# Performance work log

Measured on AMD Instinct MI355X. Metric: run time of the kernel, lower is better.

The kernel has to match this reference:

```python
import jax, jax.numpy as jnp
import numpy as np

RNN = 1024     # rnn_size
POSE = 135     # config.pose_size (15 joints x 3x3 rotmat)
SEED = 120     # seed_seq_len
TGT = 24       # target_seq_len
B = 256        # batch size


def setup_inputs() -> dict:
    key = jax.random.key(0)
    k0, k1, k2, k3, k4 = jax.random.split(key, 5)
    s = 1.0 / np.sqrt(RNN)
    poses = jax.random.normal(k0, (B, SEED + TGT, POSE), dtype=jnp.float32)
    # nn.LSTMCell(input_size, rnn_size, bias=False): weights U(-1/sqrt(H), 1/sqrt(H))
    W_ih = jax.random.uniform(k1, (4 * RNN, POSE), minval=-s, maxval=s, dtype=jnp.float32)
    W_hh = jax.random.uniform(k2, (4 * RNN, RNN), minval=-s, maxval=s, dtype=jnp.float32)
    # nn.Linear(rnn_size, pose_size)
    W_fc = jax.random.uniform(k3, (POSE, RNN), minval=-s, maxval=s, dtype=jnp.float32)
    b_fc = jax.random.uniform(k4, (POSE,), minval=-s, maxval=s, dtype=jnp.float32)
    return {"poses": poses, "W_ih": W_ih, "W_hh": W_hh, "W_fc": W_fc, "b_fc": b_fc}


def reference(poses, W_ih, W_hh, W_fc, b_fc):
    def cell(x, h, c):
        # PyTorch LSTMCell gate order: i, f, g, o ; bias=False
        gates = x @ W_ih.T + h @ W_hh.T          # [B, 4*RNN]
        i, f, g, o = jnp.split(gates, 4, axis=-1)
        c_new = jax.nn.sigmoid(f) * c + jax.nn.sigmoid(i) * jnp.tanh(g)
        h_new = jax.nn.sigmoid(o) * jnp.tanh(c_new)
        return h_new, c_new

    # Encoder: steps over poses[:, 0:SEED-1] (dropout p=0 -> identity)
    enc_inputs = jnp.transpose(poses[:, : SEED - 1], (1, 0, 2))  # [SEED-1, B, POSE]
    h0 = jnp.zeros((B, RNN), dtype=poses.dtype)
    c0 = jnp.zeros((B, RNN), dtype=poses.dtype)

    def enc_step(carry, x):
        h, c = carry
        h, c = cell(x, h, c)
        return (h, c), None

    (h, c), _ = jax.lax.scan(enc_step, (h0, c0), enc_inputs)

    # first decoder input (poses[:, SEED-1]) is ground truth. inp is detached.
    inp0 = poses[:, SEED - 1]  # [B, POSE]

    def dec_step(carry, _):
        h, c, inp = carry
        inp = jax.lax.stop_gradient(inp)  # inp.detach() in the original
        h, c = cell(inp, h, c)
        out = inp + h @ W_fc.T + b_fc     # residual + linear decode
        return (h, c, out), out

    _, outs = jax.lax.scan(dec_step, (h, c, inp0), None, length=TGT)  # [TGT, B, POSE]
    return jnp.transpose(outs, (1, 0, 2))  # predictions [B, TGT, POSE]
```

## Files before the change

### kernel.cpp

```cpp
#include <hip/hip_runtime.h>
#include <stdint.h>

#define NB 256
#define NH 1024
#define NPOSE 135
#define NPPAD 160
#define NSTEPS 143
#define NDEC 24
#define KTOT 1184
#define LSTR 168
#define NWG 256

typedef __bf16 bf16;
typedef __attribute__((ext_vector_type(8))) __bf16 bf16x8;
typedef __attribute__((ext_vector_type(4))) float f32x4;
typedef __attribute__((ext_vector_type(4))) uint32_t u32x4;

#define WCAT_OFF 0
#define WCAT_BYTES (4096l * KTOT * 2)
#define WFC_OFF  (WCAT_OFF + WCAT_BYTES)
#define WFC_BYTES (144l * 1024 * 2)
#define X_OFF    (WFC_OFF + WFC_BYTES)
#define X_BYTES  (143l * NB * NPPAD * 2)
#define H_OFF    (X_OFF + X_BYTES)
#define H_BYTES2    (2l * NB * NH * 2)
#define H_BYTES144  (144l * NB * NH * 2)
#define BAR_BYTES 16384

__device__ __forceinline__ u32x4 llc_ld16(const void* p) {
  u32x4 v;
  asm volatile("global_load_dwordx4 %0, %1, off sc0 sc1"
               : "=v"(v) : "v"(p) : "memory");
  return v;
}
__device__ __forceinline__ u32x4 g_ld16(const void* p) {
  u32x4 v;
  asm volatile("global_load_dwordx4 %0, %1, off"
               : "=v"(v) : "v"(p) : "memory");
  return v;
}
__device__ __forceinline__ u32x4 ld16sel(const void* p, bool cached) {
  return cached ? g_ld16(p) : llc_ld16(p);
}
__device__ __forceinline__ void llc_st2(void* p, uint32_t v) {
  asm volatile("global_store_short %0, %1, off sc0 sc1"
               :: "v"(p), "v"(v) : "memory");
}
#define WAIT_VM(n) do { \
    asm volatile("s_waitcnt vmcnt(" #n ")" ::: "memory"); \
    __builtin_amdgcn_sched_barrier(0); } while (0)

#define POLL(ptr, tgt) do { \
    while (__hip_atomic_load((ptr), __ATOMIC_RELAXED, __HIP_MEMORY_SCOPE_AGENT) < (tgt)) \
      __builtin_amdgcn_s_sleep(1); \
  } while (0)
#define POLL_ALL8(tgt) do { \
    for (;;) { \
      int v_ = __hip_atomic_load(&bar[(bb * 8 + (lane & 7)) * 32], \
                                 __ATOMIC_RELAXED, __HIP_MEMORY_SCOPE_AGENT); \
      if (__all(v_ >= (tgt))) break; \
      __builtin_amdgcn_s_sleep(1); \
    } } while (0)

__global__ void k_zero(uint32_t* p, int n) {
  int i = blockIdx.x * blockDim.x + threadIdx.x;
  int st = gridDim.x * blockDim.x;
  for (; i < n; i += st) p[i] = 0u;
}

__global__ void k_wcat(const float* __restrict__ Whh, const float* __restrict__ Wih,
                       bf16* __restrict__ W) {
  int n = blockIdx.x;
  for (int kk = threadIdx.x; kk < KTOT; kk += blockDim.x) {
    float v = 0.f;
    if (kk < NH) v = Whh[(size_t)n * NH + kk];
    else if (kk - NH < NPOSE) v = Wih[(size_t)n * NPOSE + (kk - NH)];
    W[(size_t)n * KTOT + kk] = (bf16)v;
  }
}

__global__ void k_wfc(const float* __restrict__ Wfc, bf16* __restrict__ W) {
  int p = blockIdx.x;
  for (int kk = threadIdx.x; kk < NH; kk += blockDim.x) {
    float v = (p < NPOSE) ? Wfc[(size_t)p * NH + kk] : 0.f;
    W[(size_t)p * NH + kk] = (bf16)v;
  }
}

__global__ void k_x(const float* __restrict__ poses, bf16* __restrict__ X) {
  int idx = blockIdx.x;
  int t = idx >> 8, b = idx & 255;
  int p = threadIdx.x;
  if (p < NPPAD) {
    float v = (p < NPOSE) ? poses[((size_t)b * 144 + t) * NPOSE + p] : 0.f;
    X[(size_t)idx * NPPAD + p] = (bf16)v;
  }
}

__device__ __forceinline__ float sigm(float x) { return 1.f / (1.f + __expf(-x)); }
__device__ __forceinline__ float tanh_(float x) {
  float e = __expf(2.f * x);
  return 1.f - 2.f / (e + 1.f);
}

template <bool DEEP>
__global__ __launch_bounds__(256, 1) void
k_main(const float* __restrict__ poses, const float* __restrict__ bfc,
       const bf16* __restrict__ Wcat, const bf16* __restrict__ Wfcb,
       bf16* __restrict__ X, bf16* __restrict__ H, int* __restrict__ bar,
       float* __restrict__ out) {
  __shared__ bf16 BldsH[8 * 64 * 128];
  __shared__ bf16 BldsX[64 * LSTR];

  const int tid  = threadIdx.x;
  const int lane = tid & 63;
  const int wv   = tid >> 6;
  const int cl   = lane & 15;
  const int quad = lane >> 4;
  const int L    = blockIdx.x;
  const int jb = (L & 7) * 8 + ((L >> 3) & 7);
  const int bb = L >> 6;
  const int b0 = bb * 64;
  const int j0 = jb * 16;
  const int mych = jb >> 3;
  const bool is_out = ((L & 7) == 7) && (((L >> 3) & 7) < 4);
  const int brow0 = bb * 64 + ((L >> 3) & 7) * 16;

  for (int t = tid; t < 8 * 64 * 16; t += 256) {
    int c = t >> 10, rem = t & 1023, r = rem >> 4, xb = rem & 15;
    u32x4 v = *(const u32x4*)&Wcat[(size_t)((r >> 4) * NH + j0 + (r & 15)) * KTOT
                                   + c * 128 + xb * 8];
    *(u32x4*)&BldsH[(c * 64 + r) * 128 + ((xb ^ (r & 15)) << 3)] = v;
  }
  for (int it = 0; it < 5; ++it) {
    int u = tid + it * 256, r = u / 20, iu = u % 20;
    u32x4 v = *(const u32x4*)&Wcat[(size_t)((r >> 4) * NH + j0 + (r & 15)) * KTOT
                                   + 1024 + iu * 8];
    *(u32x4*)&BldsX[r * LSTR + iu * 8] = v;
  }
  __syncthreads();

  const int arow = b0 + wv * 16 + cl;
  const size_t aBase  = (size_t)arow * NH + quad * 8;
  const size_t axBase = (size_t)arow * NPPAD + quad * 8;

  u32x4 A0[4], A1[4], A2[4], AX[5];
  f32x4 acc[4];
  float cst[4] = {0.f, 0.f, 0.f, 0.f};

#define ISSUE_AH(SET, HP, chn) do { \
    const bf16* ga_ = (HP) + aBase + (chn) * 128; \
    SET[0] = ld16sel(ga_, DEEP);      SET[1] = ld16sel(ga_ + 32, DEEP); \
    SET[2] = ld16sel(ga_ + 64, DEEP); SET[3] = ld16sel(ga_ + 96, DEEP); } while (0)
#define ISSUE_AX(sv) do { \
    const bf16* ga_ = X + (size_t)(sv) * NB * NPPAD + axBase; \
    if ((sv) < 120) { \
      AX[0] = g_ld16(ga_);        AX[1] = g_ld16(ga_ + 32); \
      AX[2] = g_ld16(ga_ + 64);   AX[3] = g_ld16(ga_ + 96); \
      AX[4] = g_ld16(ga_ + 128); \
    } else { \
      AX[0] = ld16sel(ga_, DEEP);       AX[1] = ld16sel(ga_ + 32, DEEP); \
      AX[2] = ld16sel(ga_ + 64, DEEP);  AX[3] = ld16sel(ga_ + 96, DEEP); \
      AX[4] = ld16sel(ga_ + 128, DEEP); \
    } } while (0)
#define MFMA_LDS(SET, c) do { \
    _Pragma("unroll") \
    for (int ks = 0; ks < 4; ++ks) { \
      bf16x8 af_ = __builtin_bit_cast(bf16x8, SET[ks]); \
      _Pragma("unroll") \
      for (int gb = 0; gb < 4; ++gb) { \
        bf16x8 bw_ = *(const bf16x8*)&BldsH[((c) * 64 + gb * 16 + cl) * 128 \
                                            + (((ks * 4 + quad) ^ cl) << 3)]; \
        acc[gb] = __builtin_amdgcn_mfma_f32_16x16x32_bf16(af_, bw_, acc[gb], 0, 0, 0); \
      } } } while (0)
#define MFMA_X() do { \
    _Pragma("unroll") \
    for (int ks = 0; ks < 5; ++ks) { \
      bf16x8 af_ = __builtin_bit_cast(bf16x8, AX[ks]); \
      _Pragma("unroll") \
      for (int gb = 0; gb < 4; ++gb) { \
        bf16x8 bw_ = *(const bf16x8*)&BldsX[(gb * 16 + cl) * LSTR + ks * 32 + quad * 8]; \
        acc[gb] = __builtin_amdgcn_mfma_f32_16x16x32_bf16(af_, bw_, acc[gb], 0, 0, 0); \
      } } } while (0)

  ISSUE_AH(A0, H, 0);
  ISSUE_AH(A1, H, 1);

  for (int s = 0; s < NSTEPS; ++s) {
    const bf16* Hr = H + (size_t)(DEEP ? s : (s & 1)) * (NB * NH);
    bf16* Hw = H + (size_t)(DEEP ? (s + 1) : ((s + 1) & 1)) * (NB * NH);
    #pragma unroll
    for (int gb = 0; gb < 4; ++gb) acc[gb] = f32x4{0, 0, 0, 0};

    ISSUE_AH(A2, Hr, 2); WAIT_VM(8); MFMA_LDS(A0, 0);
    ISSUE_AH(A0, Hr, 3); WAIT_VM(8); MFMA_LDS(A1, 1);
    ISSUE_AH(A1, Hr, 4); WAIT_VM(8); MFMA_LDS(A2, 2);
    ISSUE_AH(A2, Hr, 5); WAIT_VM(8); MFMA_LDS(A0, 3);
    ISSUE_AH(A0, Hr, 6); WAIT_VM(8); MFMA_LDS(A1, 4);
    ISSUE_AH(A1, Hr, 7); WAIT_VM(8); MFMA_LDS(A2, 5);
    if (s >= 120) POLL(&bar[(32 + bb) * 32], 4 * (s - 119));
    ISSUE_AX(s);         WAIT_VM(9); MFMA_LDS(A0, 6);
                         WAIT_VM(5); MFMA_LDS(A1, 7);
                         WAIT_VM(0); MFMA_X();

    #pragma unroll
    for (int r = 0; r < 4; ++r) {
      float gi = sigm(acc[0][r]);
      float gf = sigm(acc[1][r]);
      float gg = tanh_(acc[2][r]);
      float go = sigm(acc[3][r]);
      float cn = gf * cst[r] + gi * gg;
      cst[r] = cn;
      float h = go * tanh_(cn);
      bf16 hb = (bf16)h;
      llc_st2(&Hw[(size_t)(b0 + wv * 16 + quad * 4 + r) * NH + j0 + cl],
              (uint32_t)__builtin_bit_cast(uint16_t, hb));
    }
    WAIT_VM(0);
    __syncthreads();
    if (tid == 0) atomicAdd(&bar[(bb * 8 + mych) * 32], 1);

    if (s >= 119 && is_out) {
      const int k = s - 119;
      POLL_ALL8(8 * (s + 1));
      f32x4 oa[3] = {{0,0,0,0},{0,0,0,0},{0,0,0,0}};
      const bf16* hrow = Hw + (size_t)(brow0 + cl) * NH;
      for (int kb = 0; kb < 4; ++kb) {
        u32x4 hv[8];
        #pragma unroll
        for (int t = 0; t < 8; ++t)
          hv[t] = ld16sel(&hrow[(kb * 8 + t) * 32 + quad * 8], DEEP);
        WAIT_VM(0);
        #pragma unroll
        for (int t = 0; t < 8; ++t) {
          bf16x8 af = __builtin_bit_cast(bf16x8, hv[t]);
          #pragma unroll
          for (int i = 0; i < 3; ++i) {
            int ct = wv + i * 4;
            if (ct > 8) continue;
            bf16x8 bw = *(const bf16x8*)&Wfcb[(size_t)(ct * 16 + cl) * NH
                                              + (kb * 8 + t) * 32 + quad * 8];
            oa[i] = __builtin_amdgcn_mfma_f32_16x16x32_bf16(af, bw, oa[i], 0, 0, 0);
          }
        }
      }
      #pragma unroll
      for (int i = 0; i < 3; ++i) {
        int ct = wv + i * 4;
        if (ct > 8) continue;
        int p = ct * 16 + cl;
        if (p < NPOSE) {
          #pragma unroll
          for (int r = 0; r < 4; ++r) {
            int b = brow0 + quad * 4 + r;
            float inp = (k == 0) ? poses[((size_t)b * 144 + 119) * NPOSE + p]
                                 : out[((size_t)b * NDEC + (k - 1)) * NPOSE + p];
            float v = oa[i][r] + inp + bfc[p];
            out[((size_t)b * NDEC + k) * NPOSE + p] = v;
            if (s + 1 < NSTEPS) {
              bf16 xb = (bf16)v;
              llc_st2(&X[((size_t)(s + 1) * NB + b) * NPPAD + p],
                      (uint32_t)__builtin_bit_cast(uint16_t, xb));
            }
          }
        }
      }
      if (s + 1 < NSTEPS) {
        WAIT_VM(0);
        __syncthreads();
        if (tid == 0) atomicAdd(&bar[(32 + bb) * 32], 1);
      }
    }

    if (s + 1 < NSTEPS) {
      POLL_ALL8(8 * (s + 1));
      ISSUE_AH(A0, Hw, 0);
      ISSUE_AH(A1, Hw, 1);
    }
  }
}

extern "C" void kernel_launch(void* const* d_in, const int* in_sizes, int n_in,
                              void* d_out, int out_size, void* d_ws, size_t ws_size,
                              hipStream_t stream) {
  const float* poses = (const float*)d_in[0];
  const float* Wih   = (const float*)d_in[1];
  const float* Whh   = (const float*)d_in[2];
  const float* Wfc   = (const float*)d_in[3];
  const float* bfc   = (const float*)d_in[4];

  const size_t need_deep = (size_t)H_OFF + H_BYTES144 + BAR_BYTES;
  const size_t need_min  = (size_t)H_OFF + H_BYTES2 + BAR_BYTES;
  if (ws_size < need_min) return;
  const bool deep = ws_size >= need_deep;
  const size_t hbytes = deep ? (size_t)H_BYTES144 : (size_t)H_BYTES2;

  char* ws = (char*)d_ws;
  bf16* Wcat = (bf16*)(ws + WCAT_OFF);
  bf16* Wfcb = (bf16*)(ws + WFC_OFF);
  bf16* X    = (bf16*)(ws + X_OFF);
  bf16* H    = (bf16*)(ws + H_OFF);
  int*  bar  = (int*)(ws + H_OFF + hbytes);

  if (deep) {
    k_zero<<<256, 256, 0, stream>>>((uint32_t*)(ws + H_OFF), (int)(NB * NH * 2 / 4));
    k_zero<<<32, 256, 0, stream>>>((uint32_t*)bar, BAR_BYTES / 4);
  } else {
    k_zero<<<256, 256, 0, stream>>>((uint32_t*)(ws + H_OFF),
                                    (int)((H_BYTES2 + BAR_BYTES) / 4));
  }
  k_zero<<<256, 256, 0, stream>>>((uint32_t*)(X + (size_t)120 * NB * NPPAD),
                                  (int)(23l * NB * NPPAD * 2 / 4));
  k_wcat<<<4096, 256, 0, stream>>>(Whh, Wih, Wcat);
  k_wfc<<<144, 256, 0, stream>>>(Wfc, Wfcb);
  k_x<<<120 * 256, 256, 0, stream>>>(poses, X);
  if (deep)
    k_main<true><<<NWG, 256, 0, stream>>>(poses, bfc, Wcat, Wfcb, X, H, bar,
                                          (float*)d_out);
  else
    k_main<false><<<NWG, 256, 0, stream>>>(poses, bfc, Wcat, Wfcb, X, H, bar,
                                           (float*)d_out);
}
```

Measured before the change: 1.610 ms.

## Split K across wave pairs with LDS reduction and per-chunk barrier polling

Each wave now computes two 16-row batch tiles over half of the hidden-state K chunks, with the weight fragment as the A operand. Partial accumulators are exchanged through shared memory in four synchronized phases. Only the first half-waves run the LSTM gate math, and they write h as packed 8-byte stores instead of 2-byte shorts. Barrier polling is narrowed so each wave half waits only on the producer chunks it reads next, which lets it start prefetching sooner. The cost is extra __syncthreads, LDS traffic, and idle gate-math waves, while the per-step MFMA load is redistributed across waves.

Result: slower. 1.978 ms (+22.8%).

```diff
diff --git a/kernel.cpp b/kernel.cpp
--- a/kernel.cpp
+++ b/kernel.cpp
@@ -15,6 +15,7 @@
 typedef __attribute__((ext_vector_type(8))) __bf16 bf16x8;
 typedef __attribute__((ext_vector_type(4))) float f32x4;
 typedef __attribute__((ext_vector_type(4))) uint32_t u32x4;
+typedef __attribute__((ext_vector_type(2))) uint32_t u32x2;
 
 #define WCAT_OFF 0
 #define WCAT_BYTES (4096l * KTOT * 2)
@@ -42,8 +43,8 @@
 __device__ __forceinline__ u32x4 ld16sel(const void* p, bool cached) {
   return cached ? g_ld16(p) : llc_ld16(p);
 }
-__device__ __forceinline__ void llc_st2(void* p, uint32_t v) {
-  asm volatile("global_store_short %0, %1, off sc0 sc1"
+__device__ __forceinline__ void llc_st8(void* p, u32x2 v) {
+  asm volatile("global_store_dwordx2 %0, %1, off sc0 sc1"
                :: "v"(p), "v"(v) : "memory");
 }
 #define WAIT_VM(n) do { \
@@ -54,9 +55,9 @@
     while (__hip_atomic_load((ptr), __ATOMIC_RELAXED, __HIP_MEMORY_SCOPE_AGENT) < (tgt)) \
       __builtin_amdgcn_s_sleep(1); \
   } while (0)
-#define POLL_ALL8(tgt) do { \
+#define POLL_SET(cidx, tgt) do { \
     for (;;) { \
-      int v_ = __hip_atomic_load(&bar[(bb * 8 + (lane & 7)) * 32], \
+      int v_ = __hip_atomic_load(&bar[(bb * 8 + (cidx)) * 32], \
                                  __ATOMIC_RELAXED, __HIP_MEMORY_SCOPE_AGENT); \
       if (__all(v_ >= (tgt))) break; \
       __builtin_amdgcn_s_sleep(1); \
@@ -102,6 +103,11 @@
   float e = __expf(2.f * x);
   return 1.f - 2.f / (e + 1.f);
 }
+__device__ __forceinline__ uint32_t pack2(float a, float b) {
+  uint16_t lo = __builtin_bit_cast(uint16_t, (bf16)a);
+  uint16_t hi = __builtin_bit_cast(uint16_t, (bf16)b);
+  return ((uint32_t)hi << 16) | lo;
+}
 
 template <bool DEEP>
 __global__ __launch_bounds__(256, 1) void
@@ -111,13 +117,16 @@
        float* __restrict__ out) {
   __shared__ bf16 BldsH[8 * 64 * 128];
   __shared__ bf16 BldsX[64 * LSTR];
-
-  const int tid  = threadIdx.x;
-  const int lane = tid & 63;
-  const int wv   = tid >> 6;
-  const int cl   = lane & 15;
-  const int quad = lane >> 4;
-  const int L    = blockIdx.x;
+  __shared__ float XCH[2][64][20];
+
+  const int tid   = threadIdx.x;
+  const int lane  = tid & 63;
+  const int wv    = tid >> 6;
+  const int cl    = lane & 15;
+  const int quad  = lane >> 4;
+  const int khalf = wv >> 1;
+  const int bpair = wv & 1;
+  const int L  = blockIdx.x;
   const int jb = (L & 7) * 8 + ((L >> 3) & 7);
   const int bb = L >> 6;
   const int b0 = bb * 64;
@@ -140,89 +149,130 @@
   }
   __syncthreads();
 
-  const int arow = b0 + wv * 16 + cl;
-  const size_t aBase  = (size_t)arow * NH + quad * 8;
-  const size_t axBase = (size_t)arow * NPPAD + quad * 8;
-
-  u32x4 A0[4], A1[4], A2[4], AX[5];
-  f32x4 acc[4];
-  float cst[4] = {0.f, 0.f, 0.f, 0.f};
-
-#define ISSUE_AH(SET, HP, chn) do { \
-    const bf16* ga_ = (HP) + aBase + (chn) * 128; \
-    SET[0] = ld16sel(ga_, DEEP);      SET[1] = ld16sel(ga_ + 32, DEEP); \
-    SET[2] = ld16sel(ga_ + 64, DEEP); SET[3] = ld16sel(ga_ + 96, DEEP); } while (0)
-#define ISSUE_AX(sv) do { \
-    const bf16* ga_ = X + (size_t)(sv) * NB * NPPAD + axBase; \
+  const int arow0 = b0 + bpair * 32 + cl;
+  const size_t hB0 = (size_t)arow0 * NH + quad * 8;
+  const size_t hB1 = hB0 + (size_t)16 * NH;
+  const size_t xB0 = (size_t)arow0 * NPPAD + quad * 8;
+  const size_t xB1 = xB0 + (size_t)16 * NPPAD;
+
+  u32x4 B0[8], B1[8], B2[8], BX[10];
+  f32x4 acc[2][4];
+  float cst[8];
+  #pragma unroll
+  for (int r = 0; r < 8; ++r) cst[r] = 0.f;
+
+#define ISSUE_B(SET, HP, chn) do { \
+    const bf16* g0_ = (HP) + hB0 + (chn) * 128; \
+    const bf16* g1_ = (HP) + hB1 + (chn) * 128; \
+    SET[0] = ld16sel(g0_, DEEP);      SET[1] = ld16sel(g0_ + 32, DEEP); \
+    SET[2] = ld16sel(g0_ + 64, DEEP); SET[3] = ld16sel(g0_ + 96, DEEP); \
+    SET[4] = ld16sel(g1_, DEEP);      SET[5] = ld16sel(g1_ + 32, DEEP); \
+    SET[6] = ld16sel(g1_ + 64, DEEP); SET[7] = ld16sel(g1_ + 96, DEEP); } while (0)
+#define ISSUE_BX(sv) do { \
+    const bf16* g0_ = X + (size_t)(sv) * NB * NPPAD + xB0; \
+    const bf16* g1_ = X + (size_t)(sv) * NB * NPPAD + xB1; \
     if ((sv) < 120) { \
-      AX[0] = g_ld16(ga_);        AX[1] = g_ld16(ga_ + 32); \
-      AX[2] = g_ld16(ga_ + 64);   AX[3] = g_ld16(ga_ + 96); \
-      AX[4] = g_ld16(ga_ + 128); \
+      _Pragma("unroll") \
+      for (int k_ = 0; k_ < 5; ++k_) { BX[k_] = g_ld16(g0_ + k_ * 32); \
+                                       BX[5 + k_] = g_ld16(g1_ + k_ * 32); } \
     } else { \
-      AX[0] = ld16sel(ga_, DEEP);       AX[1] = ld16sel(ga_ + 32, DEEP); \
-      AX[2] = ld16sel(ga_ + 64, DEEP);  AX[3] = ld16sel(ga_ + 96, DEEP); \
-      AX[4] = ld16sel(ga_ + 128, DEEP); \
+      _Pragma("unroll") \
+      for (int k_ = 0; k_ < 5; ++k_) { BX[k_] = ld16sel(g0_ + k_ * 32, DEEP); \
+                                       BX[5 + k_] = ld16sel(g1_ + k_ * 32, DEEP); } \
     } } while (0)
-#define MFMA_LDS(SET, c) do { \
+#define MFMA_H(SET, c) do { \
     _Pragma("unroll") \
     for (int ks = 0; ks < 4; ++ks) { \
-      bf16x8 af_ = __builtin_bit_cast(bf16x8, SET[ks]); \
+      bf16x8 h0_ = __builtin_bit_cast(bf16x8, SET[ks]); \
+      bf16x8 h1_ = __builtin_bit_cast(bf16x8, SET[4 + ks]); \
       _Pragma("unroll") \
-      for (int gb = 0; gb < 4; ++gb) { \
-        bf16x8 bw_ = *(const bf16x8*)&BldsH[((c) * 64 + gb * 16 + cl) * 128 \
+      for (int gt = 0; gt < 4; ++gt) { \
+        bf16x8 wf_ = *(const bf16x8*)&BldsH[((c) * 64 + gt * 16 + cl) * 128 \
                                             + (((ks * 4 + quad) ^ cl) << 3)]; \
-        acc[gb] = __builtin_amdgcn_mfma_f32_16x16x32_bf16(af_, bw_, acc[gb], 0, 0, 0); \
+        acc[0][gt] = __builtin_amdgcn_mfma_f32_16x16x32_bf16(wf_, h0_, acc[0][gt], 0, 0, 0); \
+        acc[1][gt] = __builtin_amdgcn_mfma_f32_16x16x32_bf16(wf_, h1_, acc[1][gt], 0, 0, 0); \
       } } } while (0)
 #define MFMA_X() do { \
     _Pragma("unroll") \
     for (int ks = 0; ks < 5; ++ks) { \
-      bf16x8 af_ = __builtin_bit_cast(bf16x8, AX[ks]); \
+      bf16x8 h0_ = __builtin_bit_cast(bf16x8, BX[ks]); \
+      bf16x8 h1_ = __builtin_bit_cast(bf16x8, BX[5 + ks]); \
       _Pragma("unroll") \
-      for (int gb = 0; gb < 4; ++gb) { \
-        bf16x8 bw_ = *(const bf16x8*)&BldsX[(gb * 16 + cl) * LSTR + ks * 32 + quad * 8]; \
-        acc[gb] = __builtin_amdgcn_mfma_f32_16x16x32_bf16(af_, bw_, acc[gb], 0, 0, 0); \
+      for (int gt = 0; gt < 4; ++gt) { \
+        bf16x8 wf_ = *(const bf16x8*)&BldsX[(gt * 16 + cl) * LSTR + ks * 32 + quad * 8]; \
+        acc[0][gt] = __builtin_amdgcn_mfma_f32_16x16x32_bf16(wf_, h0_, acc[0][gt], 0, 0, 0); \
+        acc[1][gt] = __builtin_amdgcn_mfma_f32_16x16x32_bf16(wf_, h1_, acc[1][gt], 0, 0, 0); \
       } } } while (0)
 
-  ISSUE_AH(A0, H, 0);
-  ISSUE_AH(A1, H, 1);
+  if (khalf == 0) { ISSUE_B(B0, H, 0); ISSUE_B(B1, H, 1); }
+  else            { ISSUE_B(B0, H, 5); ISSUE_B(B1, H, 6); }
 
   for (int s = 0; s < NSTEPS; ++s) {
     const bf16* Hr = H + (size_t)(DEEP ? s : (s & 1)) * (NB * NH);
     bf16* Hw = H + (size_t)(DEEP ? (s + 1) : ((s + 1) & 1)) * (NB * NH);
     #pragma unroll
-    for (int gb = 0; gb < 4; ++gb) acc[gb] = f32x4{0, 0, 0, 0};
-
-    ISSUE_AH(A2, Hr, 2); WAIT_VM(8); MFMA_LDS(A0, 0);
-    ISSUE_AH(A0, Hr, 3); WAIT_VM(8); MFMA_LDS(A1, 1);
-    ISSUE_AH(A1, Hr, 4); WAIT_VM(8); MFMA_LDS(A2, 2);
-    ISSUE_AH(A2, Hr, 5); WAIT_VM(8); MFMA_LDS(A0, 3);
-    ISSUE_AH(A0, Hr, 6); WAIT_VM(8); MFMA_LDS(A1, 4);
-    ISSUE_AH(A1, Hr, 7); WAIT_VM(8); MFMA_LDS(A2, 5);
-    if (s >= 120) POLL(&bar[(32 + bb) * 32], 4 * (s - 119));
-    ISSUE_AX(s);         WAIT_VM(9); MFMA_LDS(A0, 6);
-                         WAIT_VM(5); MFMA_LDS(A1, 7);
-                         WAIT_VM(0); MFMA_X();
-
-    #pragma unroll
-    for (int r = 0; r < 4; ++r) {
-      float gi = sigm(acc[0][r]);
-      float gf = sigm(acc[1][r]);
-      float gg = tanh_(acc[2][r]);
-      float go = sigm(acc[3][r]);
-      float cn = gf * cst[r] + gi * gg;
-      cst[r] = cn;
-      float h = go * tanh_(cn);
-      bf16 hb = (bf16)h;
-      llc_st2(&Hw[(size_t)(b0 + wv * 16 + quad * 4 + r) * NH + j0 + cl],
-              (uint32_t)__builtin_bit_cast(uint16_t, hb));
-    }
-    WAIT_VM(0);
+    for (int bt = 0; bt < 2; ++bt)
+      #pragma unroll
+      for (int gt = 0; gt < 4; ++gt) acc[bt][gt] = f32x4{0, 0, 0, 0};
+
+    if (khalf == 0) {
+      ISSUE_B(B2, Hr, 2); WAIT_VM(16); MFMA_H(B0, 0);
+      ISSUE_B(B0, Hr, 3); WAIT_VM(16); MFMA_H(B1, 1);
+      ISSUE_B(B1, Hr, 4); WAIT_VM(16); MFMA_H(B2, 2);
+                          WAIT_VM(8);  MFMA_H(B0, 3);
+                          WAIT_VM(0);  MFMA_H(B1, 4);
+    } else {
+      ISSUE_B(B2, Hr, 7); WAIT_VM(16); MFMA_H(B0, 5);
+      if (s >= 120) POLL(&bar[(32 + bb) * 32], 4 * (s - 119));
+      ISSUE_BX(s);        WAIT_VM(18); MFMA_H(B1, 6);
+                          WAIT_VM(10); MFMA_H(B2, 7);
+                          WAIT_VM(0);  MFMA_X();
+      #pragma unroll
+      for (int gt = 0; gt < 4; ++gt)
+        *(f32x4*)&XCH[bpair][lane][gt * 4] = acc[0][gt];
+    }
     __syncthreads();
-    if (tid == 0) atomicAdd(&bar[(bb * 8 + mych) * 32], 1);
+    if (khalf == 0) {
+      #pragma unroll
+      for (int gt = 0; gt < 4; ++gt)
+        acc[0][gt] += *(const f32x4*)&XCH[bpair][lane][gt * 4];
+    }
+    __syncthreads();
+    if (khalf == 1) {
+      #pragma unroll
+      for (int gt = 0; gt < 4; ++gt)
+        *(f32x4*)&XCH[bpair][lane][gt * 4] = acc[1][gt];
+    }
+    __syncthreads();
+    if (khalf == 0) {
+      #pragma unroll
+      for (int gt = 0; gt < 4; ++gt)
+        acc[1][gt] += *(const f32x4*)&XCH[bpair][lane][gt * 4];
+    }
+    __syncthreads();
+
+    if (khalf == 0) {
+      #pragma unroll
+      for (int bt = 0; bt < 2; ++bt) {
+        float hv[4];
+        #pragma unroll
+        for (int r = 0; r < 4; ++r) {
+          float iv = acc[bt][0][r], fv = acc[bt][1][r];
+          float gv = acc[bt][2][r], ov = acc[bt][3][r];
+          float cn = sigm(fv) * cst[bt * 4 + r] + sigm(iv) * tanh_(gv);
+          cst[bt * 4 + r] = cn;
+          hv[r] = sigm(ov) * tanh_(cn);
+        }
+        u32x2 pk; pk[0] = pack2(hv[0], hv[1]); pk[1] = pack2(hv[2], hv[3]);
+        llc_st8(&Hw[(size_t)(arow0 + bt * 16) * NH + j0 + quad * 4], pk);
+      }
+      WAIT_VM(0);
+      if (lane == 0) atomicAdd(&bar[(bb * 8 + mych) * 32], 1);
+    }
 
     if (s >= 119 && is_out) {
       const int k = s - 119;
-      POLL_ALL8(8 * (s + 1));
+      POLL_SET(lane & 7, 16 * (s + 1));
       f32x4 oa[3] = {{0,0,0,0},{0,0,0,0},{0,0,0,0}};
       const bf16* hrow = Hw + (size_t)(brow0 + cl) * NH;
       for (int kb = 0; kb < 4; ++kb) {
@@ -259,8 +309,9 @@
             out[((size_t)b * NDEC + k) * NPOSE + p] = v;
             if (s + 1 < NSTEPS) {
               bf16 xb = (bf16)v;
-              llc_st2(&X[((size_t)(s + 1) * NB + b) * NPPAD + p],
-                      (uint32_t)__builtin_bit_cast(uint16_t, xb));
+              asm volatile("global_store_short %0, %1, off sc0 sc1"
+                           :: "v"(&X[((size_t)(s + 1) * NB + b) * NPPAD + p]),
+                              "v"((uint32_t)__builtin_bit_cast(uint16_t, xb)) : "memory");
             }
           }
         }
@@ -273,9 +324,16 @@
     }
 
     if (s + 1 < NSTEPS) {
-      POLL_ALL8(8 * (s + 1));
-      ISSUE_AH(A0, Hw, 0);
-      ISSUE_AH(A1, Hw, 1);
+      bf16* Hn = H + (size_t)(DEEP ? (s + 1) : ((s + 1) & 1)) * (NB * NH);
+      if (khalf == 0) {
+        int c = lane & 7; if (c > 4) c = 0;
+        POLL_SET(c, 16 * (s + 1));
+        ISSUE_B(B0, Hn, 0); ISSUE_B(B1, Hn, 1);
+      } else {
+        int c = 5 + (lane % 3);
+        POLL_SET(c, 16 * (s + 1));
+        ISSUE_B(B0, Hn, 5); ISSUE_B(B1, Hn, 6);
+      }
     }
   }
 }
```

## Switch LSTM gate GEMM to 32x32x16 MFMA with cross-wave gate exchange

Applied to the files above, without the earlier changes.

Replaces the per-wave 16x16x32 MFMA tiling (each wave covering 16 batch rows and all four gates) with 32x32x16 MFMAs. Each wave now covers 32 batch rows and two gate blocks. Gate pairs are exchanged through a small LDS buffer with an extra __syncthreads, and the cell update is done by half the waves. The aim is fewer MFMA issues and fewer LDS B-operand reads per step, but it doubles the A-register footprint, adds a block barrier per step, and serializes the nonlinearities onto two waves. The H store hint also drops sc0, which changes cache coherence behaviour for the cross-workgroup exchange.

Result: slower. 2.305 ms (+43.1%).

```diff
diff --git a/kernel.cpp b/kernel.cpp
--- a/kernel.cpp
+++ b/kernel.cpp
@@ -14,6 +14,7 @@
 typedef __bf16 bf16;
 typedef __attribute__((ext_vector_type(8))) __bf16 bf16x8;
 typedef __attribute__((ext_vector_type(4))) float f32x4;
+typedef __attribute__((ext_vector_type(16))) float f32x16;
 typedef __attribute__((ext_vector_type(4))) uint32_t u32x4;
 
 #define WCAT_OFF 0
@@ -43,7 +44,7 @@
   return cached ? g_ld16(p) : llc_ld16(p);
 }
 __device__ __forceinline__ void llc_st2(void* p, uint32_t v) {
-  asm volatile("global_store_short %0, %1, off sc0 sc1"
+  asm volatile("global_store_short %0, %1, off sc1"
                :: "v"(p), "v"(v) : "memory");
 }
 #define WAIT_VM(n) do { \
@@ -111,12 +112,19 @@
        float* __restrict__ out) {
   __shared__ bf16 BldsH[8 * 64 * 128];
   __shared__ bf16 BldsX[64 * LSTR];
+  __shared__ float XCH[2 * 64 * 18];
 
   const int tid  = threadIdx.x;
   const int lane = tid & 63;
   const int wv   = tid >> 6;
+  const int lrow = lane & 31;
+  const int half = lane >> 5;
+  const int l15  = lane & 15;
   const int cl   = lane & 15;
   const int quad = lane >> 4;
+  const int bt   = wv & 1;
+  const int ct   = wv >> 1;
+  const int ct32 = ct * 32;
   const int L    = blockIdx.x;
   const int jb = (L & 7) * 8 + ((L >> 3) & 7);
   const int bb = L >> 6;
@@ -140,48 +148,44 @@
   }
   __syncthreads();
 
-  const int arow = b0 + wv * 16 + cl;
-  const size_t aBase  = (size_t)arow * NH + quad * 8;
-  const size_t axBase = (size_t)arow * NPPAD + quad * 8;
-
-  u32x4 A0[4], A1[4], A2[4], AX[5];
-  f32x4 acc[4];
-  float cst[4] = {0.f, 0.f, 0.f, 0.f};
+  const int arow = b0 + 32 * bt + lrow;
+  const size_t aBase  = (size_t)arow * NH + half * 8;
+  const size_t axBase = (size_t)arow * NPPAD + half * 8;
+
+  u32x4 A0[8], A1[8], A2[8], AX[10];
+  f32x16 acc;
+  float cst[8];
+  #pragma unroll
+  for (int r = 0; r < 8; ++r) cst[r] = 0.f;
 
 #define ISSUE_AH(SET, HP, chn) do { \
     const bf16* ga_ = (HP) + aBase + (chn) * 128; \
-    SET[0] = ld16sel(ga_, DEEP);      SET[1] = ld16sel(ga_ + 32, DEEP); \
-    SET[2] = ld16sel(ga_ + 64, DEEP); SET[3] = ld16sel(ga_ + 96, DEEP); } while (0)
+    _Pragma("unroll") \
+    for (int kk_ = 0; kk_ < 8; ++kk_) SET[kk_] = ld16sel(ga_ + kk_ * 16, DEEP); } while (0)
 #define ISSUE_AX(sv) do { \
     const bf16* ga_ = X + (size_t)(sv) * NB * NPPAD + axBase; \
     if ((sv) < 120) { \
-      AX[0] = g_ld16(ga_);        AX[1] = g_ld16(ga_ + 32); \
-      AX[2] = g_ld16(ga_ + 64);   AX[3] = g_ld16(ga_ + 96); \
-      AX[4] = g_ld16(ga_ + 128); \
+      _Pragma("unroll") \
+      for (int kk_ = 0; kk_ < 10; ++kk_) AX[kk_] = g_ld16(ga_ + kk_ * 16); \
     } else { \
-      AX[0] = ld16sel(ga_, DEEP);       AX[1] = ld16sel(ga_ + 32, DEEP); \
-      AX[2] = ld16sel(ga_ + 64, DEEP);  AX[3] = ld16sel(ga_ + 96, DEEP); \
-      AX[4] = ld16sel(ga_ + 128, DEEP); \
+      _Pragma("unroll") \
+      for (int kk_ = 0; kk_ < 10; ++kk_) AX[kk_] = ld16sel(ga_ + kk_ * 16, DEEP); \
     } } while (0)
-#define MFMA_LDS(SET, c) do { \
+#define MFMA_H32(SET, c) do { \
     _Pragma("unroll") \
-    for (int ks = 0; ks < 4; ++ks) { \
-      bf16x8 af_ = __builtin_bit_cast(bf16x8, SET[ks]); \
-      _Pragma("unroll") \
-      for (int gb = 0; gb < 4; ++gb) { \
-        bf16x8 bw_ = *(const bf16x8*)&BldsH[((c) * 64 + gb * 16 + cl) * 128 \
-                                            + (((ks * 4 + quad) ^ cl) << 3)]; \
-        acc[gb] = __builtin_amdgcn_mfma_f32_16x16x32_bf16(af_, bw_, acc[gb], 0, 0, 0); \
-      } } } while (0)
-#define MFMA_X() do { \
+    for (int kk_ = 0; kk_ < 8; ++kk_) { \
+      bf16x8 af_ = __builtin_bit_cast(bf16x8, SET[kk_]); \
+      bf16x8 bw_ = *(const bf16x8*)&BldsH[((c) * 64 + ct32 + lrow) * 128 \
+                                          + (((kk_ * 2 + half) ^ l15) << 3)]; \
+      acc = __builtin_amdgcn_mfma_f32_32x32x16_bf16(af_, bw_, acc, 0, 0, 0); \
+    } } while (0)
+#define MFMA_X32() do { \
     _Pragma("unroll") \
-    for (int ks = 0; ks < 5; ++ks) { \
-      bf16x8 af_ = __builtin_bit_cast(bf16x8, AX[ks]); \
-      _Pragma("unroll") \
-      for (int gb = 0; gb < 4; ++gb) { \
-        bf16x8 bw_ = *(const bf16x8*)&BldsX[(gb * 16 + cl) * LSTR + ks * 32 + quad * 8]; \
-        acc[gb] = __builtin_amdgcn_mfma_f32_16x16x32_bf16(af_, bw_, acc[gb], 0, 0, 0); \
-      } } } while (0)
+    for (int kk_ = 0; kk_ < 10; ++kk_) { \
+      bf16x8 af_ = __builtin_bit_cast(bf16x8, AX[kk_]); \
+      bf16x8 bw_ = *(const bf16x8*)&BldsX[(ct32 + lrow) * LSTR + kk_ * 16 + half * 8]; \
+      acc = __builtin_amdgcn_mfma_f32_32x32x16_bf16(af_, bw_, acc, 0, 0, 0); \
+    } } while (0)
 
   ISSUE_AH(A0, H, 0);
   ISSUE_AH(A1, H, 1);
@@ -189,34 +193,54 @@
   for (int s = 0; s < NSTEPS; ++s) {
     const bf16* Hr = H + (size_t)(DEEP ? s : (s & 1)) * (NB * NH);
     bf16* Hw = H + (size_t)(DEEP ? (s + 1) : ((s + 1) & 1)) * (NB * NH);
+    acc = (f32x16)(0.f);
+
+    ISSUE_AH(A2, Hr, 2); WAIT_VM(16); MFMA_H32(A0, 0);
+    ISSUE_AH(A0, Hr, 3); WAIT_VM(16); MFMA_H32(A1, 1);
+    ISSUE_AH(A1, Hr, 4); WAIT_VM(16); MFMA_H32(A2, 2);
+    ISSUE_AH(A2, Hr, 5); WAIT_VM(16); MFMA_H32(A0, 3);
+    ISSUE_AH(A0, Hr, 6); WAIT_VM(16); MFMA_H32(A1, 4);
+    ISSUE_AH(A1, Hr, 7); WAIT_VM(16); MFMA_H32(A2, 5);
+    if (s >= 120) POLL(&bar[(32 + bb) * 32], 4 * (s - 119));
+    ISSUE_AX(s);         WAIT_VM(18); MFMA_H32(A0, 6);
+                         WAIT_VM(10); MFMA_H32(A1, 7);
+                         WAIT_VM(0);  MFMA_X32();
+
+    float va[8], vb[8];
     #pragma unroll
-    for (int gb = 0; gb < 4; ++gb) acc[gb] = f32x4{0, 0, 0, 0};
-
-    ISSUE_AH(A2, Hr, 2); WAIT_VM(8); MFMA_LDS(A0, 0);
-    ISSUE_AH(A0, Hr, 3); WAIT_VM(8); MFMA_LDS(A1, 1);
-    ISSUE_AH(A1, Hr, 4); WAIT_VM(8); MFMA_LDS(A2, 2);
-    ISSUE_AH(A2, Hr, 5); WAIT_VM(8); MFMA_LDS(A0, 3);
-    ISSUE_AH(A0, Hr, 6); WAIT_VM(8); MFMA_LDS(A1, 4);
-    ISSUE_AH(A1, Hr, 7); WAIT_VM(8); MFMA_LDS(A2, 5);
-    if (s >= 120) POLL(&bar[(32 + bb) * 32], 4 * (s - 119));
-    ISSUE_AX(s);         WAIT_VM(9); MFMA_LDS(A0, 6);
-                         WAIT_VM(5); MFMA_LDS(A1, 7);
-                         WAIT_VM(0); MFMA_X();
-
-    #pragma unroll
-    for (int r = 0; r < 4; ++r) {
-      float gi = sigm(acc[0][r]);
-      float gf = sigm(acc[1][r]);
-      float gg = tanh_(acc[2][r]);
-      float go = sigm(acc[3][r]);
-      float cn = gf * cst[r] + gi * gg;
-      cst[r] = cn;
-      float h = go * tanh_(cn);
-      bf16 hb = (bf16)h;
-      llc_st2(&Hw[(size_t)(b0 + wv * 16 + quad * 4 + r) * NH + j0 + cl],
-              (uint32_t)__builtin_bit_cast(uint16_t, hb));
-    }
-    WAIT_VM(0);
+    for (int r8i = 0; r8i < 8; ++r8i) {
+      float sa = __shfl_xor(acc[r8i], 16);
+      float sb = __shfl_xor(acc[r8i + 8], 16);
+      const bool lo = (lrow < 16);
+      va[r8i] = lo ? acc[r8i] : sb;
+      vb[r8i] = lo ? sa : acc[r8i + 8];
+    }
+    const int xbase = (bt * 64 + lane) * 18;
+    if (ct == 1) {
+      #pragma unroll
+      for (int r8i = 0; r8i < 8; ++r8i) {
+        XCH[xbase + r8i * 2]     = tanh_(va[r8i]);
+        XCH[xbase + r8i * 2 + 1] = sigm(vb[r8i]);
+      }
+    }
+    __syncthreads();
+
+    if (ct == 0) {
+      #pragma unroll
+      for (int r8i = 0; r8i < 8; ++r8i) {
+        float tg = XCH[xbase + r8i * 2];
+        float so = XCH[xbase + r8i * 2 + 1];
+        float cn = sigm(vb[r8i]) * cst[r8i] + sigm(va[r8i]) * tg;
+        cst[r8i] = cn;
+        float h = so * tanh_(cn);
+        int reg = (lrow < 16) ? r8i : (r8i + 8);
+        int row32 = (reg & 3) + 8 * (reg >> 2) + 4 * half;
+        bf16 hb = (bf16)h;
+        llc_st2(&Hw[(size_t)(b0 + 32 * bt + row32) * NH + j0 + l15],
+                (uint32_t)__builtin_bit_cast(uint16_t, hb));
+      }
+      WAIT_VM(0);
+    }
     __syncthreads();
     if (tid == 0) atomicAdd(&bar[(bb * 8 + mych) * 32], 1);
 
@@ -236,9 +260,9 @@
           bf16x8 af = __builtin_bit_cast(bf16x8, hv[t]);
           #pragma unroll
           for (int i = 0; i < 3; ++i) {
-            int ct = wv + i * 4;
-            if (ct > 8) continue;
-            bf16x8 bw = *(const bf16x8*)&Wfcb[(size_t)(ct * 16 + cl) * NH
+            int ctd = wv + i * 4;
+            if (ctd > 8) continue;
+            bf16x8 bw = *(const bf16x8*)&Wfcb[(size_t)(ctd * 16 + cl) * NH
                                               + (kb * 8 + t) * 32 + quad * 8];
             oa[i] = __builtin_amdgcn_mfma_f32_16x16x32_bf16(af, bw, oa[i], 0, 0, 0);
           }
@@ -246,9 +270,9 @@
       }
       #pragma unroll
       for (int i = 0; i < 3; ++i) {
-        int ct = wv + i * 4;
-        if (ct > 8) continue;
-        int p = ct * 16 + cl;
+        int ctd = wv + i * 4;
+        if (ctd > 8) continue;
+        int p = ctd * 16 + cl;
         if (p < NPOSE) {
           #pragma unroll
           for (int r = 0; r < 4; ++r) {
```

## Replace full step barrier with per-chunk readiness flags checked lazily

Applied to the files above, without the earlier changes.

Before, each step waited for all 8 producer chunks of the new hidden state before loading any of it. Now, in the deep-buffer path, it waits only for chunks 0 and 1. It then prefetches each later chunk's flag with an LLC-coherent load and checks it just before issuing that chunk's loads, so early MFMA work overlaps with peers still writing later chunks. This adds extra flag loads and poll loops into the MFMA pipeline and reshuffles the vmcnt waits, which could cost latency or add ordering risk. The double-buffer fallback still uses the full barrier.

Result: faster. 1.558 ms (-3.2%).

```diff
diff --git a/kernel.cpp b/kernel.cpp
--- a/kernel.cpp
+++ b/kernel.cpp
@@ -33,6 +33,12 @@
                : "=v"(v) : "v"(p) : "memory");
   return v;
 }
+__device__ __forceinline__ uint32_t llc_ld4(const void* p) {
+  uint32_t v;
+  asm volatile("global_load_dword %0, %1, off sc0 sc1"
+               : "=v"(v) : "v"(p) : "memory");
+  return v;
+}
 __device__ __forceinline__ u32x4 g_ld16(const void* p) {
   u32x4 v;
   asm volatile("global_load_dwordx4 %0, %1, off"
@@ -60,6 +66,19 @@
                                  __ATOMIC_RELAXED, __HIP_MEMORY_SCOPE_AGENT); \
       if (__all(v_ >= (tgt))) break; \
       __builtin_amdgcn_s_sleep(1); \
+    } } while (0)
+#define POLL01(tgt) do { \
+    for (;;) { \
+      int v_ = __hip_atomic_load(&bar[(bb * 8 + (lane & 1)) * 32], \
+                                 __ATOMIC_RELAXED, __HIP_MEMORY_SCOPE_AGENT); \
+      if (__all(v_ >= (tgt))) break; \
+      __builtin_amdgcn_s_sleep(1); \
+    } } while (0)
+#define CHK(fv, ch, tgt) do { \
+    while ((int)(fv) < (tgt)) { \
+      __builtin_amdgcn_s_sleep(1); \
+      fv = llc_ld4(&bar[(bb * 8 + (ch)) * 32]); \
+      WAIT_VM(0); \
     } } while (0)
 
 __global__ void k_zero(uint32_t* p, int n) {
@@ -145,9 +164,11 @@
   const size_t axBase = (size_t)arow * NPPAD + quad * 8;
 
   u32x4 A0[4], A1[4], A2[4], AX[5];
+  uint32_t f2 = 0, f3 = 0, f4 = 0, f5 = 0, f6 = 0, f7 = 0;
   f32x4 acc[4];
   float cst[4] = {0.f, 0.f, 0.f, 0.f};
 
+#define FLAGP(ch) (&bar[(bb * 8 + (ch)) * 32])
 #define ISSUE_AH(SET, HP, chn) do { \
     const bf16* ga_ = (HP) + aBase + (chn) * 128; \
     SET[0] = ld16sel(ga_, DEEP);      SET[1] = ld16sel(ga_ + 32, DEEP); \
@@ -183,25 +204,27 @@
         acc[gb] = __builtin_amdgcn_mfma_f32_16x16x32_bf16(af_, bw_, acc[gb], 0, 0, 0); \
       } } } while (0)
 
-  ISSUE_AH(A0, H, 0);
-  ISSUE_AH(A1, H, 1);
+  ISSUE_AH(A0, H, 0);  f2 = llc_ld4(FLAGP(2));
+  ISSUE_AH(A1, H, 1);  f3 = llc_ld4(FLAGP(3));
 
   for (int s = 0; s < NSTEPS; ++s) {
     const bf16* Hr = H + (size_t)(DEEP ? s : (s & 1)) * (NB * NH);
     bf16* Hw = H + (size_t)(DEEP ? (s + 1) : ((s + 1) & 1)) * (NB * NH);
     #pragma unroll
     for (int gb = 0; gb < 4; ++gb) acc[gb] = f32x4{0, 0, 0, 0};
-
-    ISSUE_AH(A2, Hr, 2); WAIT_VM(8); MFMA_LDS(A0, 0);
-    ISSUE_AH(A0, Hr, 3); WAIT_VM(8); MFMA_LDS(A1, 1);
-    ISSUE_AH(A1, Hr, 4); WAIT_VM(8); MFMA_LDS(A2, 2);
-    ISSUE_AH(A2, Hr, 5); WAIT_VM(8); MFMA_LDS(A0, 3);
-    ISSUE_AH(A0, Hr, 6); WAIT_VM(8); MFMA_LDS(A1, 4);
-    ISSUE_AH(A1, Hr, 7); WAIT_VM(8); MFMA_LDS(A2, 5);
+    const int tgt = 8 * s;
+
+    WAIT_VM(5); CHK(f2, 2, tgt); ISSUE_AH(A2, Hr, 2); f4 = llc_ld4(FLAGP(4)); MFMA_LDS(A0, 0);
+    WAIT_VM(5); CHK(f3, 3, tgt); ISSUE_AH(A0, Hr, 3); f5 = llc_ld4(FLAGP(5)); MFMA_LDS(A1, 1);
+    WAIT_VM(5); CHK(f4, 4, tgt); ISSUE_AH(A1, Hr, 4); f6 = llc_ld4(FLAGP(6)); MFMA_LDS(A2, 2);
+    WAIT_VM(5); CHK(f5, 5, tgt); ISSUE_AH(A2, Hr, 5); f7 = llc_ld4(FLAGP(7)); MFMA_LDS(A0, 3);
+    WAIT_VM(5); CHK(f6, 6, tgt); ISSUE_AH(A0, Hr, 6);                         MFMA_LDS(A1, 4);
+    WAIT_VM(4); CHK(f7, 7, tgt); ISSUE_AH(A1, Hr, 7);                         MFMA_LDS(A2, 5);
+    WAIT_VM(4);
     if (s >= 120) POLL(&bar[(32 + bb) * 32], 4 * (s - 119));
-    ISSUE_AX(s);         WAIT_VM(9); MFMA_LDS(A0, 6);
-                         WAIT_VM(5); MFMA_LDS(A1, 7);
-                         WAIT_VM(0); MFMA_X();
+    ISSUE_AX(s);                                               MFMA_LDS(A0, 6);
+    WAIT_VM(5);                                                MFMA_LDS(A1, 7);
+    WAIT_VM(0);                                                MFMA_X();
 
     #pragma unroll
     for (int r = 0; r < 4; ++r) {
@@ -273,9 +296,10 @@
     }
 
     if (s + 1 < NSTEPS) {
-      POLL_ALL8(8 * (s + 1));
-      ISSUE_AH(A0, Hw, 0);
-      ISSUE_AH(A1, Hw, 1);
+      if constexpr (DEEP) { POLL01(8 * (s + 1)); }
+      else                { POLL_ALL8(8 * (s + 1)); }
+      ISSUE_AH(A0, Hw, 0);  f2 = llc_ld4(FLAGP(2));
+      ISSUE_AH(A1, Hw, 1);  f3 = llc_ld4(FLAGP(3));
     }
   }
 }
```
